# Kernel optimization log

Measured on AMD Instinct MI355X. Metric: run time of the kernel, lower is better.

Reference implementation:

```python
import jax, jax.numpy as jnp
import numpy as np
import math

B, D, OUT = 512, 128, 100000
S, M = 32.0, 0.5
COS_M, SIN_M = math.cos(M), math.sin(M)
TH = math.cos(math.pi - M)
MM = math.sin(math.pi - M) * M
M1 = M2 = M3 = M5 = 1.0


def setup_inputs() -> dict:
    key = jax.random.key(0)
    k1, k2, k3, k4, k5, k6 = jax.random.split(key, 6)
    x = jax.random.normal(k1, (B, D), dtype=jnp.float32)
    label = jax.random.randint(k2, (B,), 0, OUT)
    k = jax.random.uniform(k3, (1, 1, 1024, 1024), dtype=jnp.float32)
    x0 = jax.random.uniform(k4, (1, 3, 112, 96), dtype=jnp.float32)
    img = jax.random.uniform(k5, (1, 3, 112, 96), dtype=jnp.float32)
    # xavier_uniform for [OUT, D]
    limit = math.sqrt(6.0 / (OUT + D))
    W = jax.random.uniform(k6, (OUT, D), minval=-limit, maxval=limit, dtype=jnp.float32)
    return {"x": x, "label": label, "k": k, "x0": x0, "img": img, "W": W}


def _arcmargin(x, W, label):
    xn = x / jnp.linalg.norm(x, axis=-1, keepdims=True)
    wn = W / jnp.linalg.norm(W, axis=-1, keepdims=True)
    cosine = xn @ wn.T                                  # [B, OUT]
    sine = jnp.sqrt(jnp.clip(1.0 - cosine * cosine, 0.0))
    phi = cosine * COS_M - sine * SIN_M
    phi = jnp.where(cosine - TH > 0, phi, cosine - MM)   # easy_margin=False
    one_hot = jax.nn.one_hot(label, OUT, dtype=cosine.dtype)
    logits = S * (one_hot * phi + (1.0 - one_hot) * cosine)
    logp = jax.nn.log_softmax(logits, axis=-1)
    return -jnp.mean(jnp.take_along_axis(logp, label[:, None], axis=1))


def _tv_loss(k):
    h, w = k.shape[-2], k.shape[-1]
    count_h = (h - 1) * w
    count_w = h * (w - 1)
    h_tv = jnp.sum((k[:, :, 1:, :] - k[:, :, :-1, :]) ** 2)
    w_tv = jnp.sum((k[:, :, :, 1:] - k[:, :, :, :-1]) ** 2)
    return -1.0 * 2.0 * (h_tv / count_h + w_tv / count_w)  # weight = -1*loss_weight


def _bin_loss(k):
    # sum over pixels of k^2 + (k-1)^2, / (h*w), then mean over batch/channel
    return jnp.mean(k * k + (k - 1.0) ** 2)


def _inv_loss(k):
    k = jax.lax.stop_gradient(k)  # original detaches before numpy FFT
    mag = jnp.abs(jnp.fft.fftn(k, axes=(-2, -1)))
    return jnp.mean(jnp.sum(mag, axis=(-1, -2)))  # L1 norm over (-1,-2), then mean


def reference(x, label, k, x0, img, W):
    loss = (M1 * _arcmargin(x, W, label)
            + M2 * _tv_loss(k)
            + M3 * _bin_loss(k)
            + M5 * _inv_loss(k))
    return loss
```

## Files before the change

kernel.cpp:

```cpp
#include <hip/hip_runtime.h>


typedef float f32x4 __attribute__((ext_vector_type(4)));
typedef unsigned short u16;
typedef unsigned int u32;
typedef unsigned long long u64;

#define BATCH 512
#define DIM 128
#define OUTN 100000
#define NOBLK 782
#define NROW2 1564
#define CHUNKS 32
#define CHSZ2 49
#define NCOL 516
#define SSCALE 32.0f
#define K2C 46.166241308446828f
#define COSM 0.8775825618903728f
#define SINM 0.479425538604203f
#define THC (-0.8775825618903728f)
#define MMC 0.2397127693021015f

#define S1_FFT 512
#define S1_XP  640
#define S1_NW  6896

#define S2_GEMM0 129
#define S2_TV0   3265
#define S2_NBLK  4289

#define GR_NBLK 66

#define DEC8(v, j) __builtin_amdgcn_cvt_f32_fp8((int)(v), (j))

__device__ inline float waveRedSum(float v) {
#pragma unroll
  for (int off = 1; off < 64; off <<= 1) v += __shfl_xor(v, off, 64);
  return v;
}

__device__ inline float quadRedSum(float v) {
#pragma unroll
  for (int off = 1; off < 16; off <<= 1) v += __shfl_xor(v, off, 64);
  return v;
}

__global__ __launch_bounds__(256) void stage1_k(const float* __restrict__ x,
                                                const float* __restrict__ W,
                                                const int* __restrict__ label,
                                                const float* __restrict__ kimg,
                                                char* __restrict__ xh8,
                                                float* __restrict__ coslab,
                                                char* __restrict__ Wh8,
                                                float2* __restrict__ fbuf,
                                                int* __restrict__ cnt) {
  __shared__ __align__(16) char smem[12288];
  int t = threadIdx.x;
  int bid = blockIdx.x;

  if (bid < S1_FFT) {
    float2* tw = (float2*)smem;
    float2* arr = (float2*)(smem + 4096);
    int r = bid;
#pragma unroll
    for (int i = 0; i < 2; i++) {
      int j = i * 256 + t;
      float s, c;
      __sincosf(-0.006135923151542565f * (float)j, &s, &c);
      tw[j] = make_float2(c, s);
    }
#pragma unroll
    for (int i = 0; i < 4; i++) {
      int idx = i * 256 + t;
      arr[idx] = make_float2(kimg[(2 * r) * 1024 + idx], kimg[(2 * r + 1) * 1024 + idx]);
    }
    __syncthreads();
    for (int lh = 9; lh >= 0; lh--) {
      int hlf = 1 << lh;
#pragma unroll
      for (int i = 0; i < 2; i++) {
        int bf = i * 256 + t;
        int pos = bf & (hlf - 1);
        int g = bf >> lh;
        int i0 = (g << (lh + 1)) + pos;
        int i1 = i0 + hlf;
        float2 u = arr[i0], v = arr[i1];
        float2 w = tw[pos << (9 - lh)];
        arr[i0] = make_float2(u.x + v.x, u.y + v.y);
        float dr = u.x - v.x, di = u.y - v.y;
        arr[i1] = make_float2(dr * w.x - di * w.y, dr * w.y + di * w.x);
      }
      __syncthreads();
    }
#pragma unroll
    for (int it = 0; it < 3; it++) {
      int k = it * 256 + t;
      if (k < NCOL) {
        float2 fa = make_float2(0.f, 0.f), fb = make_float2(0.f, 0.f);
        if (k < 513) {
          int j1 = __brev((u32)k) >> 22;
          int j2 = __brev((u32)((1024 - k) & 1023)) >> 22;
          float2 z1 = arr[j1], z2 = arr[j2];
          fa = make_float2(0.5f * (z1.x + z2.x), 0.5f * (z1.y - z2.y));
          float uu = z1.x - z2.x, vv = z1.y + z2.y;
          fb = make_float2(0.5f * vv, -0.5f * uu);
        }
        fbuf[(size_t)(2 * r) * NCOL + k] = fa;
        fbuf[(size_t)(2 * r + 1) * NCOL + k] = fb;
      }
    }
  } else if (bid < S1_XP) {
    if (bid == S1_FFT && t == 0) *cnt = 0;
    int b = (bid - S1_FFT) * 4 + (t >> 6);
    int lane = t & 63;
    size_t xb = (size_t)b * DIM;
    float2 v = *(const float2*)&x[xb + lane * 2];
    int lab = label[b];
    size_t wb = (size_t)lab * DIM;
    float2 w = *(const float2*)&W[wb + lane * 2];
    float ss = waveRedSum(v.x * v.x + v.y * v.y);
    float d  = waveRedSum(v.x * w.x + v.y * w.y);
    float nw = waveRedSum(w.x * w.x + w.y * w.y);
    float inv = rsqrtf(ss);
    u32 pk = __builtin_amdgcn_cvt_pk_fp8_f32(v.x * inv, v.y * inv, 0, 0);
    *(u16*)&xh8[b * 128 + lane * 2] = (u16)pk;
    if (lane == 0) coslab[b] = d * rsqrtf(ss * nw);
  } else {
    int row = (bid - S1_XP) * 16 + (t >> 4);
    int g16 = t & 15;
    if (row >= OUTN) {
      *(uint2*)&Wh8[(size_t)row * 128 + g16 * 8] = make_uint2(0u, 0u);
      return;
    }
    const float* wr = &W[(size_t)row * DIM + g16 * 8];
    float4 v0 = *(const float4*)wr;
    float4 v1 = *(const float4*)(wr + 4);
    float ss = quadRedSum(v0.x * v0.x + v0.y * v0.y + v0.z * v0.z + v0.w * v0.w
                        + v1.x * v1.x + v1.y * v1.y + v1.z * v1.z + v1.w * v1.w);
    float inv = rsqrtf(ss);
    u32 lo = __builtin_amdgcn_cvt_pk_fp8_f32(v0.x * inv, v0.y * inv, 0, 0);
    lo = __builtin_amdgcn_cvt_pk_fp8_f32(v0.z * inv, v0.w * inv, lo, 1);
    u32 hi = __builtin_amdgcn_cvt_pk_fp8_f32(v1.x * inv, v1.y * inv, 0, 0);
    hi = __builtin_amdgcn_cvt_pk_fp8_f32(v1.z * inv, v1.w * inv, hi, 1);
    *(uint2*)&Wh8[(size_t)row * 128 + g16 * 8] = make_uint2(lo, hi);
  }
}

__global__ __launch_bounds__(256, 4) void stage2_k(const char* __restrict__ Wh8,
                                                   const char* __restrict__ xh8,
                                                   float* __restrict__ gpart,
                                                   const float2* __restrict__ fbuf,
                                                   float* __restrict__ fftpart,
                                                   const float* __restrict__ kimg,
                                                   float4* __restrict__ tvpart) {
  __shared__ __align__(16) char smem[36880];
  int t = threadIdx.x;
  int bid = blockIdx.x;

  if (bid >= S2_TV0) {
    int r = bid - S2_TV0;
    int idx = r * 1024 + t * 4;
    float4 v = *(const float4*)&kimg[idx];
    float bs = v.x * v.x + (v.x - 1.f) * (v.x - 1.f)
             + v.y * v.y + (v.y - 1.f) * (v.y - 1.f)
             + v.z * v.z + (v.z - 1.f) * (v.z - 1.f)
             + v.w * v.w + (v.w - 1.f) * (v.w - 1.f);
    float d0 = v.y - v.x, d1 = v.z - v.y, d2 = v.w - v.z;
    float wsm = d0 * d0 + d1 * d1 + d2 * d2;
    if (t < 255) { float e4 = kimg[idx + 4]; float d3 = e4 - v.w; wsm += d3 * d3; }
    float hs = 0.f;
    if (r < 1023) {
      float4 n = *(const float4*)&kimg[idx + 1024];
      float h0 = n.x - v.x, h1 = n.y - v.y, h2 = n.z - v.z, h3 = n.w - v.w;
      hs = h0 * h0 + h1 * h1 + h2 * h2 + h3 * h3;
    }
    hs = waveRedSum(hs); wsm = waveRedSum(wsm); bs = waveRedSum(bs);
    float (*red)[4] = (float(*)[4])smem;
    if ((t & 63) == 0) { int w = t >> 6; red[0][w] = hs; red[1][w] = wsm; red[2][w] = bs; }
    __syncthreads();
    if (t == 0)
      tvpart[r] = make_float4(red[0][0] + red[0][1] + red[0][2] + red[0][3],
                              red[1][0] + red[1][1] + red[1][2] + red[1][3],
                              red[2][0] + red[2][1] + red[2][2] + red[2][3], 0.f);
  } else if (bid >= S2_GEMM0) {
    int wgrp = (bid - S2_GEMM0) & 31, g = (bid - S2_GEMM0) >> 5;
    int o = g * 8 + (wgrp & 7), bt = wgrp >> 3;
    if (o >= NOBLK) return;
    int o0 = o * 128, b0 = bt * 128;
    char* Ash = smem;
    char* Bsh = smem + 16384;
    int wv = t >> 6, lane = t & 63;
    int wo = (wv & 1) << 6, wbs = (wv >> 1) << 6;
    int m16 = lane & 15, q = lane >> 4;

    int r8 = t >> 3, cB = (t & 7) * 16, c0 = (t & 7) * 2;
#pragma unroll
    for (int it = 0; it < 4; it++) {
      int r = it * 32 + r8;
      int s = r & 15;
      uint4 va = *(const uint4*)&Wh8[(size_t)(o0 + r) * 128 + cB];
      *(u64*)&Ash[r * 128 + ((c0 ^ s) << 3)]       = ((u64)va.y << 32) | va.x;
      *(u64*)&Ash[r * 128 + (((c0 + 1) ^ s) << 3)] = ((u64)va.w << 32) | va.z;
      uint4 vb = *(const uint4*)&xh8[(size_t)(b0 + r) * 128 + cB];
      *(u64*)&Bsh[r * 128 + ((c0 ^ s) << 3)]       = ((u64)vb.y << 32) | vb.x;
      *(u64*)&Bsh[r * 128 + (((c0 + 1) ^ s) << 3)] = ((u64)vb.w << 32) | vb.z;
    }
    __syncthreads();

    f32x4 acc[4][4] = {};
#pragma unroll
    for (int kk = 0; kk < 4; kk++) {
      long af[4], bf[4];
#pragma unroll
      for (int i = 0; i < 4; i++) {
        int row = wo + i * 16 + m16;
        af[i] = *(const long*)&Ash[row * 128 + (((kk * 4 + q) ^ (row & 15)) << 3)];
      }
#pragma unroll
      for (int j = 0; j < 4; j++) {
        int row = wbs + j * 16 + m16;
        bf[j] = *(const long*)&Bsh[row * 128 + (((kk * 4 + q) ^ (row & 15)) << 3)];
      }
#pragma unroll
      for (int i = 0; i < 4; i++)
#pragma unroll
        for (int j = 0; j < 4; j++)
          acc[i][j] = __builtin_amdgcn_mfma_f32_16x16x32_fp8_fp8(af[i], bf[j], acc[i][j], 0, 0, 0);
    }
#pragma unroll
    for (int j = 0; j < 4; j++) {
      float s = 0.f;
#pragma unroll
      for (int i = 0; i < 4; i++)
#pragma unroll
        for (int r = 0; r < 4; r++)
          s += exp2f(K2C * acc[i][j][r]);
      s += __shfl_xor(s, 16, 64);
      s += __shfl_xor(s, 32, 64);
      if (q == 0)
        gpart[(size_t)(o * 2 + (wv & 1)) * 512 + b0 + wbs + j * 16 + m16] = s;
    }
  } else {
    float2* arr = (float2*)smem;
    float2* tw = (float2*)(smem + 32768);
    float* red = (float*)(smem + 36864);
    int c0 = bid * 4;
#pragma unroll
    for (int i = 0; i < 2; i++) {
      int j = i * 256 + t;
      float s, c;
      __sincosf(-0.006135923151542565f * (float)j, &s, &c);
      tw[j] = make_float2(c, s);
    }
#pragma unroll
    for (int i = 0; i < 16; i++) {
      int li = i * 256 + t;
      int rr = li >> 2, c = li & 3;
      arr[rr * 4 + c] = fbuf[(size_t)rr * NCOL + c0 + c];
    }
    __syncthreads();
    for (int lh = 9; lh >= 0; lh--) {
      int hlf = 1 << lh;
#pragma unroll
      for (int i = 0; i < 8; i++) {
        int w = i * 256 + t;
        int c = w & 3, bf = w >> 2;
        int pos = bf & (hlf - 1), g2i = bf >> lh;
        int i0 = ((g2i << (lh + 1)) + pos) * 4 + c;
        int i1 = i0 + hlf * 4;
        float2 u = arr[i0], v = arr[i1];
        float2 tww = tw[pos << (9 - lh)];
        arr[i0] = make_float2(u.x + v.x, u.y + v.y);
        float dr = u.x - v.x, di = u.y - v.y;
        arr[i1] = make_float2(dr * tww.x - di * tww.y, dr * tww.y + di * tww.x);
      }
      __syncthreads();
    }
    float s = 0.f;
#pragma unroll
    for (int i = 0; i < 16; i++) {
      int li = i * 256 + t;
      int col = c0 + (li & 3);
      float w = (col == 0 || col == 512) ? 1.f : (col < 512 ? 2.f : 0.f);
      float2 v = arr[li];
      s += w * sqrtf(v.x * v.x + v.y * v.y);
    }
    s = waveRedSum(s);
    if ((t & 63) == 0) red[t >> 6] = s;
    __syncthreads();
    if (t == 0) fftpart[bid] = red[0] + red[1] + red[2] + red[3];
  }
}

__global__ __launch_bounds__(256) void gemmred_k(const float* __restrict__ gpart,
                                                 float* __restrict__ g2,
                                                 const char* __restrict__ xh8,
                                                 const char* __restrict__ Wh8,
                                                 const int* __restrict__ label,
                                                 float* __restrict__ labexp,
                                                 const float* __restrict__ coslab,
                                                 const float4* __restrict__ tvpart,
                                                 const float* __restrict__ fftpart,
                                                 int* __restrict__ cnt,
                                                 float* __restrict__ out) {
  int t = threadIdx.x;
  int blk = blockIdx.x;
  if (blk < 64) {
    int chunk = blk >> 1, half = blk & 1;
    int b = half * 256 + t;
    int rBeg = chunk * CHSZ2;
    int rEnd = rBeg + CHSZ2; if (rEnd > NROW2) rEnd = NROW2;
    float s = 0.f;
    for (int r = rBeg; r < rEnd; r++) s += gpart[(size_t)r * 512 + b];
    g2[chunk * 512 + b] = s;
  } else {
    int b = (blk - 64) * 256 + t;
    int lab = label[b];
    const u32* xr = (const u32*)(xh8 + (size_t)b * 128);
    const u32* wr = (const u32*)(Wh8 + (size_t)lab * 128);
    float d = 0.f;
#pragma unroll 4
    for (int i = 0; i < 32; i++) {
      u32 xa = xr[i], wa = wr[i];
      d += DEC8(xa, 0) * DEC8(wa, 0) + DEC8(xa, 1) * DEC8(wa, 1)
         + DEC8(xa, 2) * DEC8(wa, 2) + DEC8(xa, 3) * DEC8(wa, 3);
    }
    labexp[b] = exp2f(K2C * d);
  }

  __shared__ int lastFlag;
  __threadfence();
  __syncthreads();
  if (t == 0) lastFlag = (atomicAdd(cnt, 1) == GR_NBLK - 1);
  __syncthreads();
  if (!lastFlag) return;
  __threadfence();

  float arc = 0.f, hs = 0.f, wsm = 0.f, bs = 0.f, fs = 0.f;
#pragma unroll
  for (int i = 0; i < 2; i++) {
    int b = i * 256 + t;
    float se = 0.f;
#pragma unroll
    for (int c = 0; c < CHUNKS; c++) se += g2[c * 512 + b];
    se -= 96.0f;
    se -= labexp[b];
    float cl = coslab[b];
    float sine = sqrtf(fmaxf(0.f, 1.f - cl * cl));
    float phi = cl * COSM - sine * SINM;
    if (!(cl - THC > 0.f)) phi = cl - MMC;
    arc += __logf(se + exp2f(K2C * phi)) - SSCALE * phi;
  }
#pragma unroll
  for (int i = 0; i < 4; i++) {
    float4 p = tvpart[i * 256 + t];
    hs += p.x; wsm += p.y; bs += p.z;
  }
  fs = (t < S2_GEMM0) ? fftpart[t] : 0.f;
  arc = waveRedSum(arc); hs = waveRedSum(hs); wsm = waveRedSum(wsm);
  bs = waveRedSum(bs); fs = waveRedSum(fs);
  __shared__ float red[5][4];
  if ((t & 63) == 0) {
    int w = t >> 6;
    red[0][w] = arc; red[1][w] = hs; red[2][w] = wsm; red[3][w] = bs; red[4][w] = fs;
  }
  __syncthreads();
  if (t == 0) {
    float A = 0, H = 0, Wv = 0, Bv = 0, F = 0;
#pragma unroll
    for (int w = 0; w < 4; w++) {
      A += red[0][w]; H += red[1][w]; Wv += red[2][w]; Bv += red[3][w]; F += red[4][w];
    }
    float cnt2 = 1023.0f * 1024.0f;
    out[0] = A * (1.0f / 512.0f) - 2.0f * (H / cnt2 + Wv / cnt2)
           + Bv * (1.0f / 1048576.0f) + F;
  }
}

extern "C" void kernel_launch(void* const* d_in, const int* in_sizes, int n_in,
                              void* d_out, int out_size, void* d_ws, size_t ws_size,
                              hipStream_t stream) {
  const float* x = (const float*)d_in[0];
  const int* label = (const int*)d_in[1];
  const float* kimg = (const float*)d_in[2];
  const float* W = (const float*)d_in[5];
  float* out = (float*)d_out;
  char* ws = (char*)d_ws;
  float*  coslab  = (float*)(ws + 0);
  char*   xh8     = (char*)(ws + 2048);
  char*   Wh8     = (char*)(ws + 67584);
  float2* fbuf    = (float2*)(ws + 12879872);
  float*  gpart   = (float*)(ws + 17106944);
  float*  g2      = (float*)(ws + 20310016);
  float4* tvpart  = (float4*)(ws + 20375552);
  float*  fftpart = (float*)(ws + 20391936);
  float*  labexp  = (float*)(ws + 20393984);
  int*    cnt     = (int*)(ws + 20396032);

  hipLaunchKernelGGL(stage1_k, dim3(S1_NW), dim3(256), 0, stream,
                     x, W, label, kimg, xh8, coslab, Wh8, fbuf, cnt);
  hipLaunchKernelGGL(stage2_k, dim3(S2_NBLK), dim3(256), 0, stream,
                     Wh8, xh8, gpart, fbuf, fftpart, kimg, tvpart);
  hipLaunchKernelGGL(gemmred_k, dim3(GR_NBLK), dim3(256), 0, stream,
                     gpart, g2, xh8, Wh8, label, labexp,
                     coslab, tvpart, fftpart, cnt, out);
}
```

Baseline: 141.0 us.

## Fuse TV/binary loss into FFT blocks and process two W rows per thread

The TV and binary-loss reduction moves out of separate stage-2 blocks and into the stage-1 FFT blocks. Those blocks already load pairs of image rows, so the loss reuses those loads plus one extra row read and the LDS copy for the horizontal differences. The W normalisation/fp8 conversion now handles two rows per thread, which halves that block count. Together these cut extra launch blocks and a second full read of the image, at the cost of more work and registers in the FFT blocks and one extra syncthreads.

```diff
diff --git a/kernel.cpp b/kernel.cpp
--- a/kernel.cpp
+++ b/kernel.cpp
@@ -23,11 +23,10 @@
 
 #define S1_FFT 512
 #define S1_XP  640
-#define S1_NW  6896
+#define S1_NW  3768
 
 #define S2_GEMM0 129
-#define S2_TV0   3265
-#define S2_NBLK  4289
+#define S2_NBLK  3265
 
 #define GR_NBLK 66
 
@@ -53,15 +52,18 @@
                                                 float* __restrict__ coslab,
                                                 char* __restrict__ Wh8,
                                                 float2* __restrict__ fbuf,
+                                                float4* __restrict__ tvpart,
                                                 int* __restrict__ cnt) {
-  __shared__ __align__(16) char smem[12288];
+  __shared__ __align__(16) char smem[12352];
   int t = threadIdx.x;
   int bid = blockIdx.x;
 
   if (bid < S1_FFT) {
     float2* tw = (float2*)smem;
     float2* arr = (float2*)(smem + 4096);
+    float (*red)[4] = (float(*)[4])(smem + 12288);
     int r = bid;
+    float hs = 0.f, wsm = 0.f, bs = 0.f;
 #pragma unroll
     for (int i = 0; i < 2; i++) {
       int j = i * 256 + t;
@@ -72,7 +74,25 @@
 #pragma unroll
     for (int i = 0; i < 4; i++) {
       int idx = i * 256 + t;
-      arr[idx] = make_float2(kimg[(2 * r) * 1024 + idx], kimg[(2 * r + 1) * 1024 + idx]);
+      float va = kimg[(2 * r) * 1024 + idx];
+      float vb = kimg[(2 * r + 1) * 1024 + idx];
+      arr[idx] = make_float2(va, vb);
+      bs += va * va + (va - 1.f) * (va - 1.f) + vb * vb + (vb - 1.f) * (vb - 1.f);
+      float dv = vb - va; hs += dv * dv;
+      if (r < 511) {
+        float vc = kimg[(2 * r + 2) * 1024 + idx];
+        float dc = vc - vb; hs += dc * dc;
+      }
+    }
+    __syncthreads();
+#pragma unroll
+    for (int i = 0; i < 4; i++) {
+      int idx = i * 256 + t;
+      if (idx < 1023) {
+        float2 a = arr[idx], b2 = arr[idx + 1];
+        float dx = b2.x - a.x, dy = b2.y - a.y;
+        wsm += dx * dx + dy * dy;
+      }
     }
     __syncthreads();
     for (int lh = 9; lh >= 0; lh--) {
@@ -109,6 +129,13 @@
         fbuf[(size_t)(2 * r + 1) * NCOL + k] = fb;
       }
     }
+    hs = waveRedSum(hs); wsm = waveRedSum(wsm); bs = waveRedSum(bs);
+    if ((t & 63) == 0) { int w = t >> 6; red[0][w] = hs; red[1][w] = wsm; red[2][w] = bs; }
+    __syncthreads();
+    if (t == 0)
+      tvpart[r] = make_float4(red[0][0] + red[0][1] + red[0][2] + red[0][3],
+                              red[1][0] + red[1][1] + red[1][2] + red[1][3],
+                              red[2][0] + red[2][1] + red[2][2] + red[2][3], 0.f);
   } else if (bid < S1_XP) {
     if (bid == S1_FFT && t == 0) *cnt = 0;
     int b = (bid - S1_FFT) * 4 + (t >> 6);
@@ -126,23 +153,34 @@
     *(u16*)&xh8[b * 128 + lane * 2] = (u16)pk;
     if (lane == 0) coslab[b] = d * rsqrtf(ss * nw);
   } else {
-    int row = (bid - S1_XP) * 16 + (t >> 4);
+    int rA = (bid - S1_XP) * 32 + (t >> 4) * 2;
     int g16 = t & 15;
-    if (row >= OUTN) {
-      *(uint2*)&Wh8[(size_t)row * 128 + g16 * 8] = make_uint2(0u, 0u);
+    if (rA >= OUTN) {
+      *(uint2*)&Wh8[(size_t)rA * 128 + g16 * 8] = make_uint2(0u, 0u);
+      *(uint2*)&Wh8[(size_t)(rA + 1) * 128 + g16 * 8] = make_uint2(0u, 0u);
       return;
     }
-    const float* wr = &W[(size_t)row * DIM + g16 * 8];
-    float4 v0 = *(const float4*)wr;
-    float4 v1 = *(const float4*)(wr + 4);
-    float ss = quadRedSum(v0.x * v0.x + v0.y * v0.y + v0.z * v0.z + v0.w * v0.w
-                        + v1.x * v1.x + v1.y * v1.y + v1.z * v1.z + v1.w * v1.w);
-    float inv = rsqrtf(ss);
-    u32 lo = __builtin_amdgcn_cvt_pk_fp8_f32(v0.x * inv, v0.y * inv, 0, 0);
-    lo = __builtin_amdgcn_cvt_pk_fp8_f32(v0.z * inv, v0.w * inv, lo, 1);
-    u32 hi = __builtin_amdgcn_cvt_pk_fp8_f32(v1.x * inv, v1.y * inv, 0, 0);
-    hi = __builtin_amdgcn_cvt_pk_fp8_f32(v1.z * inv, v1.w * inv, hi, 1);
-    *(uint2*)&Wh8[(size_t)row * 128 + g16 * 8] = make_uint2(lo, hi);
+    const float* wrA = &W[(size_t)rA * DIM + g16 * 8];
+    const float* wrB = &W[(size_t)(rA + 1) * DIM + g16 * 8];
+    float4 a0 = *(const float4*)wrA;
+    float4 a1 = *(const float4*)(wrA + 4);
+    float4 b0 = *(const float4*)wrB;
+    float4 b1 = *(const float4*)(wrB + 4);
+    float ssA = quadRedSum(a0.x * a0.x + a0.y * a0.y + a0.z * a0.z + a0.w * a0.w
+                         + a1.x * a1.x + a1.y * a1.y + a1.z * a1.z + a1.w * a1.w);
+    float ssB = quadRedSum(b0.x * b0.x + b0.y * b0.y + b0.z * b0.z + b0.w * b0.w
+                         + b1.x * b1.x + b1.y * b1.y + b1.z * b1.z + b1.w * b1.w);
+    float invA = rsqrtf(ssA), invB = rsqrtf(ssB);
+    u32 lo = __builtin_amdgcn_cvt_pk_fp8_f32(a0.x * invA, a0.y * invA, 0, 0);
+    lo = __builtin_amdgcn_cvt_pk_fp8_f32(a0.z * invA, a0.w * invA, lo, 1);
+    u32 hi = __builtin_amdgcn_cvt_pk_fp8_f32(a1.x * invA, a1.y * invA, 0, 0);
+    hi = __builtin_amdgcn_cvt_pk_fp8_f32(a1.z * invA, a1.w * invA, hi, 1);
+    *(uint2*)&Wh8[(size_t)rA * 128 + g16 * 8] = make_uint2(lo, hi);
+    lo = __builtin_amdgcn_cvt_pk_fp8_f32(b0.x * invB, b0.y * invB, 0, 0);
+    lo = __builtin_amdgcn_cvt_pk_fp8_f32(b0.z * invB, b0.w * invB, lo, 1);
+    hi = __builtin_amdgcn_cvt_pk_fp8_f32(b1.x * invB, b1.y * invB, 0, 0);
+    hi = __builtin_amdgcn_cvt_pk_fp8_f32(b1.z * invB, b1.w * invB, hi, 1);
+    *(uint2*)&Wh8[(size_t)(rA + 1) * 128 + g16 * 8] = make_uint2(lo, hi);
   }
 }
 
@@ -150,39 +188,12 @@
                                                    const char* __restrict__ xh8,
                                                    float* __restrict__ gpart,
                                                    const float2* __restrict__ fbuf,
-                                                   float* __restrict__ fftpart,
-                                                   const float* __restrict__ kimg,
-                                                   float4* __restrict__ tvpart) {
+                                                   float* __restrict__ fftpart) {
   __shared__ __align__(16) char smem[36880];
   int t = threadIdx.x;
   int bid = blockIdx.x;
 
-  if (bid >= S2_TV0) {
-    int r = bid - S2_TV0;
-    int idx = r * 1024 + t * 4;
-    float4 v = *(const float4*)&kimg[idx];
-    float bs = v.x * v.x + (v.x - 1.f) * (v.x - 1.f)
-             + v.y * v.y + (v.y - 1.f) * (v.y - 1.f)
-             + v.z * v.z + (v.z - 1.f) * (v.z - 1.f)
-             + v.w * v.w + (v.w - 1.f) * (v.w - 1.f);
-    float d0 = v.y - v.x, d1 = v.z - v.y, d2 = v.w - v.z;
-    float wsm = d0 * d0 + d1 * d1 + d2 * d2;
-    if (t < 255) { float e4 = kimg[idx + 4]; float d3 = e4 - v.w; wsm += d3 * d3; }
-    float hs = 0.f;
-    if (r < 1023) {
-      float4 n = *(const float4*)&kimg[idx + 1024];
-      float h0 = n.x - v.x, h1 = n.y - v.y, h2 = n.z - v.z, h3 = n.w - v.w;
-      hs = h0 * h0 + h1 * h1 + h2 * h2 + h3 * h3;
-    }
-    hs = waveRedSum(hs); wsm = waveRedSum(wsm); bs = waveRedSum(bs);
-    float (*red)[4] = (float(*)[4])smem;
-    if ((t & 63) == 0) { int w = t >> 6; red[0][w] = hs; red[1][w] = wsm; red[2][w] = bs; }
-    __syncthreads();
-    if (t == 0)
-      tvpart[r] = make_float4(red[0][0] + red[0][1] + red[0][2] + red[0][3],
-                              red[1][0] + red[1][1] + red[1][2] + red[1][3],
-                              red[2][0] + red[2][1] + red[2][2] + red[2][3], 0.f);
-  } else if (bid >= S2_GEMM0) {
+  if (bid >= S2_GEMM0) {
     int wgrp = (bid - S2_GEMM0) & 31, g = (bid - S2_GEMM0) >> 5;
     int o = g * 8 + (wgrp & 7), bt = wgrp >> 3;
     if (o >= NOBLK) return;
@@ -352,7 +363,7 @@
     arc += __logf(se + exp2f(K2C * phi)) - SSCALE * phi;
   }
 #pragma unroll
-  for (int i = 0; i < 4; i++) {
+  for (int i = 0; i < 2; i++) {
     float4 p = tvpart[i * 256 + t];
     hs += p.x; wsm += p.y; bs += p.z;
   }
@@ -393,14 +404,14 @@
   float*  gpart   = (float*)(ws + 17106944);
   float*  g2      = (float*)(ws + 20310016);
   float4* tvpart  = (float4*)(ws + 20375552);
-  float*  fftpart = (float*)(ws + 20391936);
-  float*  labexp  = (float*)(ws + 20393984);
-  int*    cnt     = (int*)(ws + 20396032);
+  float*  fftpart = (float*)(ws + 20383744);
+  float*  labexp  = (float*)(ws + 20385792);
+  int*    cnt     = (int*)(ws + 20387840);
 
   hipLaunchKernelGGL(stage1_k, dim3(S1_NW), dim3(256), 0, stream,
-                     x, W, label, kimg, xh8, coslab, Wh8, fbuf, cnt);
+                     x, W, label, kimg, xh8, coslab, Wh8, fbuf, tvpart, cnt);
   hipLaunchKernelGGL(stage2_k, dim3(S2_NBLK), dim3(256), 0, stream,
-                     Wh8, xh8, gpart, fbuf, fftpart, kimg, tvpart);
+                     Wh8, xh8, gpart, fbuf, fftpart);
   hipLaunchKernelGGL(gemmred_k, dim3(GR_NBLK), dim3(256), 0, stream,
                      gpart, g2, xh8, Wh8, label, labexp,
                      coslab, tvpart, fftpart, cnt, out);
```

After: 143.2 us. Within noise of the previous version (+1.6%).
